# Optimization experiments

Hardware: AMD Instinct MI355X
Metric: run time of the kernel (lower is better)

The kernel has to match this reference:

```python
import jax, jax.numpy as jnp
import numpy as np

# DCNV3_YOLO config: inc==ouc=128 (no stem_conv), k=3, s=1, pad=autopad(3)=1, g=4, d=1, SiLU act
N, C, H, W = 4, 128, 96, 96
G = 4
GC = C // G          # group channels = 32
K = 3                # dcn kernel (also depthwise conv kernel)
PAD = 1
P = K * K            # sampling points per group
EPS = 1e-5


def setup_inputs() -> dict:
    key = jax.random.key(0)
    ks = jax.random.split(key, 8)
    d = {}
    d["x"] = jax.random.normal(ks[0], (N, C, H, W), jnp.float32)
    # DCNv3 params (torch Linear weight (out,in) -> stored transposed (in,out) here)
    d["dw_w"] = jax.random.normal(ks[1], (C, 1, K, K), jnp.float32) * 0.1  # depthwise conv
    d["dw_b"] = jnp.zeros((C,), jnp.float32)
    d["ln_g"] = jnp.ones((C,), jnp.float32)   # LN inside dw_conv branch
    d["ln_b"] = jnp.zeros((C,), jnp.float32)
    d["w_off"] = jax.random.normal(ks[2], (C, G * P * 2), jnp.float32) * 0.01
    d["b_off"] = jnp.zeros((G * P * 2,), jnp.float32)
    d["w_mask"] = jax.random.normal(ks[3], (C, G * P), jnp.float32) * 0.02
    d["b_mask"] = jnp.zeros((G * P,), jnp.float32)
    d["w_in"] = jax.random.normal(ks[4], (C, C), jnp.float32) * (1.0 / np.sqrt(C))
    d["b_in"] = jnp.zeros((C,), jnp.float32)
    d["w_out"] = jax.random.normal(ks[5], (C, C), jnp.float32) * (1.0 / np.sqrt(C))
    d["b_out"] = jnp.zeros((C,), jnp.float32)
    # BatchNorm2d (eval mode: running stats)
    d["bn_g"] = jnp.ones((C,), jnp.float32)
    d["bn_b"] = jnp.zeros((C,), jnp.float32)
    d["bn_mean"] = jnp.zeros((C,), jnp.float32)
    d["bn_var"] = jnp.ones((C,), jnp.float32)
    return d


def _dcnv3_core(xp, offset, mask):
    # xp: (N,H,W,C) projected input; offset: (N,H,W,G*P*2); mask: (N,H,W,G,P) softmaxed
    n, h, w, _ = xp.shape
    xpad = jnp.pad(xp, ((0, 0), (PAD, PAD), (PAD, PAD), (0, 0)))
    H_in, W_in = h + 2 * PAD, w + 2 * PAD
    Ho, Wo = h, w  # stride 1, k=3, pad=1 -> same spatial size
    # reference points (pixel centers in padded frame, normalized), matches _get_reference_points
    base = (K - 1) // 2 + 0.5  # 1.5
    ref_y = (jnp.arange(Ho, dtype=jnp.float32) + base) / H_in
    ref_x = (jnp.arange(Wo, dtype=jnp.float32) + base) / W_in
    # dilation grid; torch flattens meshgrid(x_lin, y_lin) ij -> x outer, y inner
    lin = jnp.arange(K, dtype=jnp.float32) - (K - 1) // 2  # [-1,0,1]
    gx, gy = jnp.meshgrid(lin, lin, indexing='ij')  # (K,K), x varies along axis 0
    gridx = (gx / W_in).reshape(P)
    gridy = (gy / H_in).reshape(P)
    off = offset.reshape(n, Ho, Wo, G, P, 2)
    # normalized sampling locations (offset_scale = 1.0)
    loc_x = ref_x[None, None, :, None, None] + gridx[None, None, None, None, :] + off[..., 0] / W_in
    loc_y = ref_y[None, :, None, None, None] + gridy[None, None, None, None, :] + off[..., 1] / H_in
    # grid_sample(align_corners=False) unnormalize of (2*loc-1): loc*size - 0.5
    ix = (loc_x * W_in - 0.5).transpose(0, 3, 1, 2, 4)  # (N,G,Ho,Wo,P)
    iy = (loc_y * H_in - 0.5).transpose(0, 3, 1, 2, 4)
    x0 = jnp.floor(ix); y0 = jnp.floor(iy)
    wx1 = ix - x0; wx0 = 1.0 - wx1
    wy1 = iy - y0; wy0 = 1.0 - wy1
    x0i = x0.astype(jnp.int32); y0i = y0.astype(jnp.int32)
    x1i = x0i + 1; y1i = y0i + 1
    img = xpad.reshape(n, H_in * W_in, G, GC).transpose(0, 2, 1, 3)  # (N,G,S,GC)

    def samp(yi, xi, wgt):
        valid = (yi >= 0) & (yi < H_in) & (xi >= 0) & (xi < W_in)  # zeros padding
        idx = jnp.clip(yi, 0, H_in - 1) * W_in + jnp.clip(xi, 0, W_in - 1)
        idxf = idx.reshape(n, G, Ho * Wo * P, 1)
        v = jnp.take_along_axis(img, idxf, axis=2)  # (N,G,Ho*Wo*P,GC)
        w_eff = jnp.where(valid, wgt, 0.0).reshape(n, G, Ho * Wo * P, 1)
        return v * w_eff

    val = (samp(y0i, x0i, wy0 * wx0) + samp(y0i, x1i, wy0 * wx1)
           + samp(y1i, x0i, wy1 * wx0) + samp(y1i, x1i, wy1 * wx1))
    val = val.reshape(n, G, Ho, Wo, P, GC)
    m = mask.transpose(0, 3, 1, 2, 4)[..., None]  # (N,G,Ho,Wo,P,1)
    out = (val * m).sum(axis=4)  # (N,G,Ho,Wo,GC)
    return out.transpose(0, 2, 3, 1, 4).reshape(n, Ho, Wo, G * GC)


def reference(x, dw_w, dw_b, ln_g, ln_b, w_off, b_off, w_mask, b_mask,
              w_in, b_in, w_out, b_out, bn_g, bn_b, bn_mean, bn_var):
    x_nhwc = x.transpose(0, 2, 3, 1)  # NCHW -> NHWC
    x_proj = x_nhwc @ w_in + b_in     # input_proj
    # dw_conv branch: depthwise conv -> LayerNorm(channels_last) -> GELU
    x1 = jax.lax.conv_general_dilated(x, dw_w, (1, 1), ((PAD, PAD), (PAD, PAD)),
                                      feature_group_count=C,
                                      dimension_numbers=('NCHW', 'OIHW', 'NCHW'))
    x1 = x1.transpose(0, 2, 3, 1) + dw_b
    mu = x1.mean(-1, keepdims=True)
    var = ((x1 - mu) ** 2).mean(-1, keepdims=True)
    x1 = (x1 - mu) * jax.lax.rsqrt(var + EPS) * ln_g + ln_b
    x1 = jax.nn.gelu(x1, approximate=False)
    offset = x1 @ w_off + b_off  # (N,H,W,G*P*2)
    mask = jax.nn.softmax((x1 @ w_mask + b_mask).reshape(N, H, W, G, P), axis=-1)
    out = _dcnv3_core(x_proj, offset, mask)
    out = out @ w_out + b_out    # output_proj
    y = out.transpose(0, 3, 1, 2)  # back to NCHW
    # BatchNorm2d (eval) + SiLU
    inv = jax.lax.rsqrt(bn_var + EPS)
    y = (y - bn_mean[:, None, None]) * (inv * bn_g)[:, None, None] + bn_b[:, None, None]
    return y * jax.nn.sigmoid(y)
```

## Files before the change

kernel.cpp:

```cpp
#include <hip/hip_runtime.h>
#include <math.h>

#define NN 4
#define CCH 128
#define HH 96
#define WW 96
#define SS (HH*WW)
#define GG 4
#define GC 32
#define PP 9
#define NPIX (NN*HH*WW)

typedef short bf16x8 __attribute__((ext_vector_type(8)));
typedef float f32x4 __attribute__((ext_vector_type(4)));
typedef unsigned short u16;
typedef unsigned int u32;

static __device__ __forceinline__ u16 f2bf(float f) {
  unsigned u = __builtin_bit_cast(unsigned, f);
  unsigned r = (u + 0x7fffu + ((u >> 16) & 1u)) >> 16;
  return (u16)r;
}
static __device__ __forceinline__ float bflo(u32 u) {
  return __builtin_bit_cast(float, u << 16);
}
static __device__ __forceinline__ float bfhi(u32 u) {
  return __builtin_bit_cast(float, u & 0xffff0000u);
}

__global__ __launch_bounds__(128) void k_prep(const float* __restrict__ w_in,
    const float* __restrict__ w_off, const float* __restrict__ w_mask,
    const float* __restrict__ w_out, const float* __restrict__ dw_w,
    u16* __restrict__ w_inT, u16* __restrict__ w_omT, u16* __restrict__ w_outT,
    u16* __restrict__ dw_wT) {
  int r = blockIdx.x, k = threadIdx.x;
  if (r < 128) {
    w_inT[r*128 + k] = f2bf(w_in[k*128 + r]);
  } else if (r < 240) {
    int c = r - 128;
    float v = 0.f;
    if (c < 72) v = w_off[k*72 + c];
    else if (c < 108) v = w_mask[k*36 + (c - 72)];
    w_omT[c*128 + k] = f2bf(v);
  } else if (r < 368) {
    int c = r - 240;
    w_outT[c*128 + k] = f2bf(w_out[k*128 + c]);
  } else {
    int j = r - 368;
    dw_wT[j*128 + k] = f2bf(dw_w[k*9 + j]);
  }
}

__global__ __launch_bounds__(256) void k_tr_in(const float* __restrict__ x,
                                               u16* __restrict__ xTb) {
  __shared__ float tile[32][132];
  int n = blockIdx.z;
  int cs = blockIdx.y * 32;
  int ps = blockIdx.x * 128;
  int t = threadIdx.x;
  const float* src = x + ((size_t)n*CCH + cs)*SS + ps;
  #pragma unroll
  for (int i = 0; i < 4; ++i) {
    int f = t + i*256;
    int row = f >> 5, col4 = f & 31;
    float4 v = *(const float4*)(src + (size_t)row*SS + col4*4);
    *(float4*)&tile[row][col4*4] = v;
  }
  __syncthreads();
  u16* dst = xTb + ((size_t)n*SS + ps)*CCH + cs;
  #pragma unroll
  for (int i = 0; i < 8; ++i) {
    int gidx = t + i*256;
    int px = gidx >> 4, cp = gidx & 15;
    u32 pk = (u32)f2bf(tile[cp*2][px]) | ((u32)f2bf(tile[cp*2+1][px]) << 16);
    *(u32*)(dst + (size_t)px*CCH + cp*2) = pk;
  }
}

__global__ __launch_bounds__(64) void k_proj16(const u16* __restrict__ xTb,
    const u16* __restrict__ wT, const float* __restrict__ bias,
    u16* __restrict__ xpb) {
  int l = threadIdx.x;
  int c16 = l & 15, kq = l >> 4;
  int px0 = blockIdx.x * 16;
  const u16* arow = xTb + (size_t)(px0 + c16)*CCH + kq*8;
  bf16x8 a[4];
  #pragma unroll
  for (int ks = 0; ks < 4; ++ks) a[ks] = *(const bf16x8*)(arow + ks*32);
  f32x4 acc[8] = {};
  #pragma unroll
  for (int ks = 0; ks < 4; ++ks) {
    #pragma unroll
    for (int nt = 0; nt < 8; ++nt) {
      bf16x8 b = *(const bf16x8*)(wT + (size_t)(nt*16 + c16)*CCH + ks*32 + kq*8);
      acc[nt] = __builtin_amdgcn_mfma_f32_16x16x32_bf16(a[ks], b, acc[nt], 0, 0, 0);
    }
  }
  #pragma unroll
  for (int nt = 0; nt < 8; ++nt) {
    int c = nt*16 + c16;
    float bs = bias[c];
    #pragma unroll
    for (int r = 0; r < 4; ++r)
      xpb[(size_t)(px0 + kq*4 + r)*CCH + c] = f2bf(acc[nt][r] + bs);
  }
}

__global__ __launch_bounds__(256) void k_dwom(const u16* __restrict__ xTb,
    const u16* __restrict__ dw_wT, const float* __restrict__ dw_b,
    const float* __restrict__ ln_g, const float* __restrict__ ln_b,
    const u16* __restrict__ wTom, const float* __restrict__ b_off,
    const float* __restrict__ b_mask,
    float* __restrict__ off, float* __restrict__ mask) {
  __shared__ u16 x1t[16][136];
  __shared__ float msk[16][40];
  int t = threadIdx.x;
  int blk = blockIdx.x;
  const int W16 = WW/16;
  int w0 = (blk % W16) * 16;
  int h  = (blk / W16) % HH;
  int n  = blk / (W16*HH);
  size_t pix0 = (size_t)n*SS + (size_t)h*WW + w0;

  {
    int px = t >> 4, cg = t & 15;
    int w = w0 + px;
    int c0 = cg * 8;
    const u16* src = xTb + (size_t)n*SS*CCH + c0;
    float wtv[9][8];
    #pragma unroll
    for (int j = 0; j < 9; ++j) {
      bf16x8 wr = *(const bf16x8*)(dw_wT + j*CCH + c0);
      u32 uw[4]; *(bf16x8*)uw = wr;
      #pragma unroll
      for (int q = 0; q < 4; ++q) { wtv[j][2*q] = bflo(uw[q]); wtv[j][2*q+1] = bfhi(uw[q]); }
    }
    float s8[8] = {};
    #pragma unroll
    for (int kh = 0; kh < 3; ++kh) {
      int yy = h - 1 + kh;
      if (yy < 0 || yy >= HH) continue;
      #pragma unroll
      for (int kw = 0; kw < 3; ++kw) {
        int xx = w - 1 + kw;
        if (xx < 0 || xx >= WW) continue;
        bf16x8 raw = *(const bf16x8*)(src + (size_t)(yy*WW + xx)*CCH);
        u32 uw[4]; *(bf16x8*)uw = raw;
        #pragma unroll
        for (int q = 0; q < 4; ++q) {
          s8[2*q]   = fmaf(bflo(uw[q]), wtv[kh*3+kw][2*q],   s8[2*q]);
          s8[2*q+1] = fmaf(bfhi(uw[q]), wtv[kh*3+kw][2*q+1], s8[2*q+1]);
        }
      }
    }
    float4 db0 = *(const float4*)(dw_b + c0);
    float4 db1 = *(const float4*)(dw_b + c0 + 4);
    s8[0]+=db0.x; s8[1]+=db0.y; s8[2]+=db0.z; s8[3]+=db0.w;
    s8[4]+=db1.x; s8[5]+=db1.y; s8[6]+=db1.z; s8[7]+=db1.w;
    float s1 = 0.f, s2 = 0.f;
    #pragma unroll
    for (int j = 0; j < 8; ++j) { s1 += s8[j]; s2 += s8[j]*s8[j]; }
    #pragma unroll
    for (int m = 8; m >= 1; m >>= 1) {
      s1 += __shfl_xor(s1, m);
      s2 += __shfl_xor(s2, m);
    }
    float mean = s1 * (1.f/128.f);
    float var  = s2 * (1.f/128.f) - mean*mean;
    float rstd = rsqrtf(var + 1e-5f);
    float4 lg0 = *(const float4*)(ln_g + c0);
    float4 lg1 = *(const float4*)(ln_g + c0 + 4);
    float4 lb0 = *(const float4*)(ln_b + c0);
    float4 lb1 = *(const float4*)(ln_b + c0 + 4);
    float lg[8] = {lg0.x,lg0.y,lg0.z,lg0.w,lg1.x,lg1.y,lg1.z,lg1.w};
    float lb[8] = {lb0.x,lb0.y,lb0.z,lb0.w,lb1.x,lb1.y,lb1.z,lb1.w};
    u32 pk[4];
    #pragma unroll
    for (int q = 0; q < 4; ++q) {
      float v0 = (s8[2*q]   - mean) * rstd * lg[2*q]   + lb[2*q];
      float v1 = (s8[2*q+1] - mean) * rstd * lg[2*q+1] + lb[2*q+1];
      float g0 = 0.5f * v0 * (1.f + erff(v0 * 0.70710678f));
      float g1 = 0.5f * v1 * (1.f + erff(v1 * 0.70710678f));
      pk[q] = (u32)f2bf(g0) | ((u32)f2bf(g1) << 16);
    }
    *(bf16x8*)&x1t[px][c0] = *(bf16x8*)pk;
  }
  __syncthreads();

  {
    int wv = t >> 6, l = t & 63, c16 = l & 15, kq = l >> 4;
    int nt0 = wv*2;
    int ntn = (wv == 3) ? 1 : 2;
    f32x4 acc[2] = {};
    #pragma unroll
    for (int ks = 0; ks < 4; ++ks) {
      bf16x8 a = *(const bf16x8*)&x1t[c16][kq*8 + ks*32];
      #pragma unroll
      for (int j = 0; j < 2; ++j) {
        if (j < ntn) {
          bf16x8 b = *(const bf16x8*)(wTom + (size_t)((nt0+j)*16 + c16)*CCH + ks*32 + kq*8);
          acc[j] = __builtin_amdgcn_mfma_f32_16x16x32_bf16(a, b, acc[j], 0, 0, 0);
        }
      }
    }
    #pragma unroll
    for (int j = 0; j < 2; ++j) {
      if (j < ntn) {
        int c = (nt0+j)*16 + c16;
        float bs = (c < 72) ? b_off[c] : ((c < 108) ? b_mask[c - 72] : 0.f);
        #pragma unroll
        for (int r = 0; r < 4; ++r) {
          int px = kq*4 + r;
          float v = acc[j][r] + bs;
          if (c < 72) off[(pix0 + px)*72 + c] = v;
          else if (c < 108) msk[px][c - 72] = v;
        }
      }
    }
  }
  __syncthreads();

  if (t < 64) {
    int px = t >> 2, g = t & 3;
    float mx = -1e30f;
    #pragma unroll
    for (int q = 0; q < PP; ++q) mx = fmaxf(mx, msk[px][g*PP + q]);
    float e[PP]; float sum = 0.f;
    #pragma unroll
    for (int q = 0; q < PP; ++q) { e[q] = __expf(msk[px][g*PP + q] - mx); sum += e[q]; }
    float inv = 1.f / sum;
    #pragma unroll
    for (int q = 0; q < PP; ++q)
      mask[(pix0 + px)*36 + g*PP + q] = e[q] * inv;
  }
}

__global__ __launch_bounds__(256) void k_dcnout(const u16* __restrict__ xpb,
    const float* __restrict__ off, const float* __restrict__ mask,
    const u16* __restrict__ wTout, const float* __restrict__ b_out,
    const float* __restrict__ bn_g, const float* __restrict__ bn_b,
    const float* __restrict__ bn_mean, const float* __restrict__ bn_var,
    float* __restrict__ y) {
  __shared__ float smem[16*132];
  __shared__ u16 dtile[16][136];
  float (*offs)[72] = (float(*)[72])smem;
  float (*ms)[36]   = (float(*)[36])(smem + 16*72);
  int t = threadIdx.x;
  int pb = blockIdx.x * 16;
  {
    const float* po = off + (size_t)pb*72;
    #pragma unroll
    for (int i = 0; i < 5; ++i) {
      int idx = t + i*256;
      if (idx < 16*72) smem[idx] = po[idx];
    }
    const float* pm = mask + (size_t)pb*36;
    #pragma unroll
    for (int i = 0; i < 3; ++i) {
      int idx = t + i*256;
      if (idx < 16*36) smem[16*72 + idx] = pm[idx];
    }
  }
  __syncthreads();

  {
    int pxl = t >> 4, unit = t & 15;
    int g = unit >> 2, ch0 = unit * 8;
    int pix = pb + pxl;
    int w = pix % WW; int h = (pix / WW) % HH; int n = pix / SS;
    const u16* basep = xpb + (size_t)n*SS*CCH + ch0;
    float a8[8] = {};
    #pragma unroll
    for (int bt = 0; bt < 3; ++bt) {
      bf16x8 raw[3][4];
      float wgt[3][4];
      float mv[3];
      #pragma unroll
      for (int q = 0; q < 3; ++q) {
        int p = bt*3 + q;
        float offx = offs[pxl][(g*PP + p)*2 + 0];
        float offy = offs[pxl][(g*PP + p)*2 + 1];
        mv[q] = ms[pxl][g*PP + p];
        float ix = (float)w + 1.0f + (float)(p / 3 - 1) + offx;
        float iy = (float)h + 1.0f + (float)(p % 3 - 1) + offy;
        float x0f = floorf(ix), y0f = floorf(iy);
        float wx1 = ix - x0f, wx0 = 1.f - wx1;
        float wy1 = iy - y0f, wy0 = 1.f - wy1;
        int x0i = (int)x0f, y0i = (int)y0f;
        int ox0 = x0i - 1, oy0 = y0i - 1;
        int ox1 = x0i,     oy1 = y0i;
        bool y0ok = (oy0 >= 0) & (oy0 < HH), y1ok = (oy1 >= 0) & (oy1 < HH);
        bool x0ok = (ox0 >= 0) & (ox0 < WW), x1ok = (ox1 >= 0) & (ox1 < WW);
        int cy0 = min(max(oy0, 0), HH-1), cy1 = min(max(oy1, 0), HH-1);
        int cx0 = min(max(ox0, 0), WW-1), cx1 = min(max(ox1, 0), WW-1);
        wgt[q][0] = (y0ok & x0ok) ? wy0*wx0 : 0.f;
        wgt[q][1] = (y0ok & x1ok) ? wy0*wx1 : 0.f;
        wgt[q][2] = (y1ok & x0ok) ? wy1*wx0 : 0.f;
        wgt[q][3] = (y1ok & x1ok) ? wy1*wx1 : 0.f;
        raw[q][0] = *(const bf16x8*)(basep + (size_t)(cy0*WW + cx0)*CCH);
        raw[q][1] = *(const bf16x8*)(basep + (size_t)(cy0*WW + cx1)*CCH);
        raw[q][2] = *(const bf16x8*)(basep + (size_t)(cy1*WW + cx0)*CCH);
        raw[q][3] = *(const bf16x8*)(basep + (size_t)(cy1*WW + cx1)*CCH);
      }
      #pragma unroll
      for (int q = 0; q < 3; ++q) {
        float v8[8] = {};
        #pragma unroll
        for (int corner = 0; corner < 4; ++corner) {
          u32 uw[4]; *(bf16x8*)uw = raw[q][corner];
          float wg = wgt[q][corner];
          #pragma unroll
          for (int j = 0; j < 4; ++j) {
            v8[2*j]   = fmaf(wg, bflo(uw[j]), v8[2*j]);
            v8[2*j+1] = fmaf(wg, bfhi(uw[j]), v8[2*j+1]);
          }
        }
        #pragma unroll
        for (int j = 0; j < 8; ++j) a8[j] = fmaf(mv[q], v8[j], a8[j]);
      }
    }
    u32 pk[4];
    #pragma unroll
    for (int j = 0; j < 4; ++j)
      pk[j] = (u32)f2bf(a8[2*j]) | ((u32)f2bf(a8[2*j+1]) << 16);
    *(bf16x8*)&dtile[pxl][ch0] = *(bf16x8*)pk;
  }
  __syncthreads();

  {
    int wv = t >> 6, l = t & 63, c16 = l & 15, kq = l >> 4;
    f32x4 acc[2] = {};
    #pragma unroll
    for (int ks = 0; ks < 4; ++ks) {
      bf16x8 a = *(const bf16x8*)&dtile[c16][kq*8 + ks*32];
      #pragma unroll
      for (int j = 0; j < 2; ++j) {
        int nt = wv*2 + j;
        bf16x8 b = *(const bf16x8*)(wTout + (size_t)(nt*16 + c16)*CCH + ks*32 + kq*8);
        acc[j] = __builtin_amdgcn_mfma_f32_16x16x32_bf16(a, b, acc[j], 0, 0, 0);
      }
    }
    float (*fout)[132] = (float(*)[132])smem;
    #pragma unroll
    for (int j = 0; j < 2; ++j) {
      int c = (wv*2 + j)*16 + c16;
      float sc = rsqrtf(bn_var[c] + 1e-5f) * bn_g[c];
      float sh = bn_b[c] - bn_mean[c] * sc;
      float bs = b_out[c];
      #pragma unroll
      for (int r = 0; r < 4; ++r) {
        int px = kq*4 + r;
        float v = (acc[j][r] + bs) * sc + sh;
        float sig = 1.f / (1.f + __expf(-v));
        fout[px][c] = v * sig;
      }
    }
  }
  __syncthreads();

  {
    float (*fout)[132] = (float(*)[132])smem;
    int n = pb / SS, rem = pb % SS;
    float* dst = y + ((size_t)n*CCH)*SS + rem;
    #pragma unroll
    for (int i = 0; i < 2; ++i) {
      int id = t + i*256;
      int c = id >> 2, p4 = (id & 3) * 4;
      float4 v = { fout[p4][c], fout[p4+1][c], fout[p4+2][c], fout[p4+3][c] };
      *(float4*)(dst + (size_t)c*SS + p4) = v;
    }
  }
}

extern "C" void kernel_launch(void* const* d_in, const int* in_sizes, int n_in,
                              void* d_out, int out_size, void* d_ws, size_t ws_size,
                              hipStream_t stream) {
  const float* x       = (const float*)d_in[0];
  const float* dw_w    = (const float*)d_in[1];
  const float* dw_b    = (const float*)d_in[2];
  const float* ln_g    = (const float*)d_in[3];
  const float* ln_b    = (const float*)d_in[4];
  const float* w_off   = (const float*)d_in[5];
  const float* b_off   = (const float*)d_in[6];
  const float* w_mask  = (const float*)d_in[7];
  const float* b_mask  = (const float*)d_in[8];
  const float* w_in    = (const float*)d_in[9];
  const float* b_in    = (const float*)d_in[10];
  const float* w_out   = (const float*)d_in[11];
  const float* b_out   = (const float*)d_in[12];
  const float* bn_g    = (const float*)d_in[13];
  const float* bn_b    = (const float*)d_in[14];
  const float* bn_mean = (const float*)d_in[15];
  const float* bn_var  = (const float*)d_in[16];
  float* y = (float*)d_out;

  u16*  xTb  = (u16*)d_ws;
  u16*  xpb  = xTb + (size_t)NPIX*CCH;
  float* offb = (float*)(xpb + (size_t)NPIX*CCH);
  float* mb   = offb + (size_t)NPIX*72;
  u16*  wbuf  = (u16*)(mb + (size_t)NPIX*36);
  u16*  w_inT  = wbuf;
  u16*  w_omT  = w_inT + 128*128;
  u16*  w_outT = w_omT + 112*128;
  u16*  dw_wTb = w_outT + 128*128;

  dim3 trg(SS/128, CCH/32, NN);
  k_prep<<<377, 128, 0, stream>>>(w_in, w_off, w_mask, w_out, dw_w,
                                  w_inT, w_omT, w_outT, dw_wTb);
  k_tr_in<<<trg, 256, 0, stream>>>(x, xTb);
  k_proj16<<<NPIX/16, 64, 0, stream>>>(xTb, w_inT, b_in, xpb);
  k_dwom<<<NPIX/16, 256, 0, stream>>>(xTb, dw_wTb, dw_b, ln_g, ln_b,
                                      w_omT, b_off, b_mask, offb, mb);
  k_dcnout<<<NPIX/16, 256, 0, stream>>>(xpb, offb, mb, w_outT, b_out,
                                        bn_g, bn_b, bn_mean, bn_var, y);
}
```

Before: 179.3 us.

## Stage a 5x20 halo tile of projected input in LDS for bilinear sampling

```diff
diff --git a/kernel.cpp b/kernel.cpp
--- a/kernel.cpp
+++ b/kernel.cpp
@@ -243,10 +243,15 @@
     float* __restrict__ y) {
   __shared__ float smem[16*132];
   __shared__ u16 dtile[16][136];
+  __shared__ u16 halo[5*20*128];
   float (*offs)[72] = (float(*)[72])smem;
   float (*ms)[36]   = (float(*)[36])(smem + 16*72);
   int t = threadIdx.x;
   int pb = blockIdx.x * 16;
+  int n = pb / SS, rem = pb % SS;
+  int h = rem / WW, w0 = rem % WW;
+  const u16* xpimg = xpb + (size_t)n*SS*CCH;
+
   {
     const float* po = off + (size_t)pb*72;
     #pragma unroll
@@ -260,63 +265,64 @@
       int idx = t + i*256;
       if (idx < 16*36) smem[16*72 + idx] = pm[idx];
     }
+    for (int i = t; i < 1600; i += 256) {
+      int pxl = i >> 4, seg = i & 15;
+      int r = pxl / 20, c = pxl - r*20;
+      int gy = min(max(h - 2 + r, 0), HH-1);
+      int gx = min(max(w0 - 2 + c, 0), WW-1);
+      *(bf16x8*)&halo[(size_t)i*8] =
+          *(const bf16x8*)(xpimg + (size_t)(gy*WW + gx)*CCH + seg*8);
+    }
   }
   __syncthreads();
 
   {
     int pxl = t >> 4, unit = t & 15;
     int g = unit >> 2, ch0 = unit * 8;
-    int pix = pb + pxl;
-    int w = pix % WW; int h = (pix / WW) % HH; int n = pix / SS;
-    const u16* basep = xpb + (size_t)n*SS*CCH + ch0;
+    int w = w0 + pxl;
     float a8[8] = {};
     #pragma unroll
-    for (int bt = 0; bt < 3; ++bt) {
-      bf16x8 raw[3][4];
-      float wgt[3][4];
-      float mv[3];
-      #pragma unroll
-      for (int q = 0; q < 3; ++q) {
-        int p = bt*3 + q;
-        float offx = offs[pxl][(g*PP + p)*2 + 0];
-        float offy = offs[pxl][(g*PP + p)*2 + 1];
-        mv[q] = ms[pxl][g*PP + p];
-        float ix = (float)w + 1.0f + (float)(p / 3 - 1) + offx;
-        float iy = (float)h + 1.0f + (float)(p % 3 - 1) + offy;
-        float x0f = floorf(ix), y0f = floorf(iy);
-        float wx1 = ix - x0f, wx0 = 1.f - wx1;
-        float wy1 = iy - y0f, wy0 = 1.f - wy1;
-        int x0i = (int)x0f, y0i = (int)y0f;
-        int ox0 = x0i - 1, oy0 = y0i - 1;
-        int ox1 = x0i,     oy1 = y0i;
-        bool y0ok = (oy0 >= 0) & (oy0 < HH), y1ok = (oy1 >= 0) & (oy1 < HH);
-        bool x0ok = (ox0 >= 0) & (ox0 < WW), x1ok = (ox1 >= 0) & (ox1 < WW);
-        int cy0 = min(max(oy0, 0), HH-1), cy1 = min(max(oy1, 0), HH-1);
-        int cx0 = min(max(ox0, 0), WW-1), cx1 = min(max(ox1, 0), WW-1);
-        wgt[q][0] = (y0ok & x0ok) ? wy0*wx0 : 0.f;
-        wgt[q][1] = (y0ok & x1ok) ? wy0*wx1 : 0.f;
-        wgt[q][2] = (y1ok & x0ok) ? wy1*wx0 : 0.f;
-        wgt[q][3] = (y1ok & x1ok) ? wy1*wx1 : 0.f;
-        raw[q][0] = *(const bf16x8*)(basep + (size_t)(cy0*WW + cx0)*CCH);
-        raw[q][1] = *(const bf16x8*)(basep + (size_t)(cy0*WW + cx1)*CCH);
-        raw[q][2] = *(const bf16x8*)(basep + (size_t)(cy1*WW + cx0)*CCH);
-        raw[q][3] = *(const bf16x8*)(basep + (size_t)(cy1*WW + cx1)*CCH);
-      }
-      #pragma unroll
-      for (int q = 0; q < 3; ++q) {
-        float v8[8] = {};
+    for (int p = 0; p < PP; ++p) {
+      float offx = offs[pxl][(g*PP + p)*2 + 0];
+      float offy = offs[pxl][(g*PP + p)*2 + 1];
+      float mval = ms[pxl][g*PP + p];
+      float ix = (float)w + 1.0f + (float)(p / 3 - 1) + offx;
+      float iy = (float)h + 1.0f + (float)(p % 3 - 1) + offy;
+      float x0f = floorf(ix), y0f = floorf(iy);
+      float wx1 = ix - x0f, wx0 = 1.f - wx1;
+      float wy1 = iy - y0f, wy0 = 1.f - wy1;
+      int x0i = (int)x0f, y0i = (int)y0f;
+      int ox0 = x0i - 1, oy0 = y0i - 1;
+      int ox1 = x0i,     oy1 = y0i;
+      bool y0ok = (oy0 >= 0) & (oy0 < HH), y1ok = (oy1 >= 0) & (oy1 < HH);
+      bool x0ok = (ox0 >= 0) & (ox0 < WW), x1ok = (ox1 >= 0) & (ox1 < WW);
+      float cw[4];
+      cw[0] = ((y0ok & x0ok) ? wy0*wx0 : 0.f) * mval;
+      cw[1] = ((y0ok & x1ok) ? wy0*wx1 : 0.f) * mval;
+      cw[2] = ((y1ok & x0ok) ? wy1*wx0 : 0.f) * mval;
+      cw[3] = ((y1ok & x1ok) ? wy1*wx1 : 0.f) * mval;
+      int ly0 = oy0 - h + 2, lx0 = ox0 - w0 + 2;
+      #pragma unroll
+      for (int corner = 0; corner < 4; ++corner) {
+        int ly = ly0 + (corner >> 1);
+        int lx = lx0 + (corner & 1);
+        float wg = cw[corner];
+        bf16x8 raw;
+        if ((u32)ly < 5u && (u32)lx < 20u) {
+          raw = *(const bf16x8*)&halo[(size_t)(ly*20 + lx)*128 + ch0];
+        } else {
+          int oy = (corner < 2) ? oy0 : oy0 + 1;
+          int ox = (corner & 1) ? ox0 + 1 : ox0;
+          int cy = min(max(oy, 0), HH-1);
+          int cx = min(max(ox, 0), WW-1);
+          raw = *(const bf16x8*)(xpimg + (size_t)(cy*WW + cx)*CCH + ch0);
+        }
+        u32 uw[4]; *(bf16x8*)uw = raw;
         #pragma unroll
-        for (int corner = 0; corner < 4; ++corner) {
-          u32 uw[4]; *(bf16x8*)uw = raw[q][corner];
-          float wg = wgt[q][corner];
-          #pragma unroll
-          for (int j = 0; j < 4; ++j) {
-            v8[2*j]   = fmaf(wg, bflo(uw[j]), v8[2*j]);
-            v8[2*j+1] = fmaf(wg, bfhi(uw[j]), v8[2*j+1]);
-          }
+        for (int j = 0; j < 4; ++j) {
+          a8[2*j]   = fmaf(wg, bflo(uw[j]), a8[2*j]);
+          a8[2*j+1] = fmaf(wg, bfhi(uw[j]), a8[2*j+1]);
         }
-        #pragma unroll
-        for (int j = 0; j < 8; ++j) a8[j] = fmaf(mv[q], v8[j], a8[j]);
       }
     }
     u32 pk[4];
@@ -360,7 +366,6 @@
 
   {
     float (*fout)[132] = (float(*)[132])smem;
-    int n = pb / SS, rem = pb % SS;
     float* dst = y + ((size_t)n*CCH)*SS + rem;
     #pragma unroll
     for (int i = 0; i < 2; ++i) {
```

After: 194.6 us. 8.5% more time.

## Fuse NCHW transpose with input projection GEMM and fold mask into bilinear weights

Applied to the files above, without the earlier changes.

```diff
diff --git a/kernel.cpp b/kernel.cpp
--- a/kernel.cpp
+++ b/kernel.cpp
@@ -51,58 +51,63 @@
   }
 }
 
-__global__ __launch_bounds__(256) void k_tr_in(const float* __restrict__ x,
-                                               u16* __restrict__ xTb) {
-  __shared__ float tile[32][132];
-  int n = blockIdx.z;
-  int cs = blockIdx.y * 32;
-  int ps = blockIdx.x * 128;
+__global__ __launch_bounds__(256) void k_trproj(const float* __restrict__ x,
+    const u16* __restrict__ wT, const float* __restrict__ bias,
+    u16* __restrict__ xTb, u16* __restrict__ xpb) {
+  __shared__ u16 tile[32][136];
   int t = threadIdx.x;
-  const float* src = x + ((size_t)n*CCH + cs)*SS + ps;
+  int pb = blockIdx.x * 32;
+  int n = pb / SS, ps = pb % SS;
+  const float* src = x + ((size_t)n*CCH)*SS + ps;
+
   #pragma unroll
   for (int i = 0; i < 4; ++i) {
-    int f = t + i*256;
-    int row = f >> 5, col4 = f & 31;
-    float4 v = *(const float4*)(src + (size_t)row*SS + col4*4);
-    *(float4*)&tile[row][col4*4] = v;
-  }
-  __syncthreads();
-  u16* dst = xTb + ((size_t)n*SS + ps)*CCH + cs;
-  #pragma unroll
-  for (int i = 0; i < 8; ++i) {
-    int gidx = t + i*256;
-    int px = gidx >> 4, cp = gidx & 15;
-    u32 pk = (u32)f2bf(tile[cp*2][px]) | ((u32)f2bf(tile[cp*2+1][px]) << 16);
-    *(u32*)(dst + (size_t)px*CCH + cp*2) = pk;
-  }
-}
-
-__global__ __launch_bounds__(64) void k_proj16(const u16* __restrict__ xTb,
-    const u16* __restrict__ wT, const float* __restrict__ bias,
-    u16* __restrict__ xpb) {
-  int l = threadIdx.x;
-  int c16 = l & 15, kq = l >> 4;
-  int px0 = blockIdx.x * 16;
-  const u16* arow = xTb + (size_t)(px0 + c16)*CCH + kq*8;
-  bf16x8 a[4];
-  #pragma unroll
-  for (int ks = 0; ks < 4; ++ks) a[ks] = *(const bf16x8*)(arow + ks*32);
-  f32x4 acc[8] = {};
-  #pragma unroll
-  for (int ks = 0; ks < 4; ++ks) {
-    #pragma unroll
-    for (int nt = 0; nt < 8; ++nt) {
-      bf16x8 b = *(const bf16x8*)(wT + (size_t)(nt*16 + c16)*CCH + ks*32 + kq*8);
-      acc[nt] = __builtin_amdgcn_mfma_f32_16x16x32_bf16(a[ks], b, acc[nt], 0, 0, 0);
-    }
-  }
-  #pragma unroll
-  for (int nt = 0; nt < 8; ++nt) {
-    int c = nt*16 + c16;
-    float bs = bias[c];
-    #pragma unroll
-    for (int r = 0; r < 4; ++r)
-      xpb[(size_t)(px0 + kq*4 + r)*CCH + c] = f2bf(acc[nt][r] + bs);
+    int fid = t + i*256;
+    int c = fid >> 3, q = fid & 7;
+    float4 v = *(const float4*)(src + (size_t)c*SS + q*4);
+    int px = q*4;
+    tile[px+0][c] = f2bf(v.x);
+    tile[px+1][c] = f2bf(v.y);
+    tile[px+2][c] = f2bf(v.z);
+    tile[px+3][c] = f2bf(v.w);
+  }
+  __syncthreads();
+
+  {
+    u32* dst = (u32*)(xTb + (size_t)pb*CCH);
+    #pragma unroll
+    for (int i = 0; i < 8; ++i) {
+      int gidx = t + i*256;
+      int px = gidx >> 6, cp = gidx & 63;
+      dst[(size_t)px*64 + cp] = *(const u32*)&tile[px][cp*2];
+    }
+  }
+
+  {
+    int wv = t >> 6, l = t & 63, c16 = l & 15, kq = l >> 4;
+    int pxl0 = (wv & 1) * 16;
+    int nt0 = (wv >> 1) * 4;
+    bf16x8 a[4];
+    #pragma unroll
+    for (int ks = 0; ks < 4; ++ks)
+      a[ks] = *(const bf16x8*)&tile[pxl0 + c16][kq*8 + ks*32];
+    f32x4 acc[4] = {};
+    #pragma unroll
+    for (int ks = 0; ks < 4; ++ks) {
+      #pragma unroll
+      for (int j = 0; j < 4; ++j) {
+        bf16x8 b = *(const bf16x8*)(wT + (size_t)((nt0+j)*16 + c16)*CCH + ks*32 + kq*8);
+        acc[j] = __builtin_amdgcn_mfma_f32_16x16x32_bf16(a[ks], b, acc[j], 0, 0, 0);
+      }
+    }
+    #pragma unroll
+    for (int j = 0; j < 4; ++j) {
+      int c = (nt0+j)*16 + c16;
+      float bs = bias[c];
+      #pragma unroll
+      for (int r = 0; r < 4; ++r)
+        xpb[(size_t)(pb + pxl0 + kq*4 + r)*CCH + c] = f2bf(acc[j][r] + bs);
+    }
   }
 }
 
@@ -274,13 +279,12 @@
     for (int bt = 0; bt < 3; ++bt) {
       bf16x8 raw[3][4];
       float wgt[3][4];
-      float mv[3];
       #pragma unroll
       for (int q = 0; q < 3; ++q) {
         int p = bt*3 + q;
         float offx = offs[pxl][(g*PP + p)*2 + 0];
         float offy = offs[pxl][(g*PP + p)*2 + 1];
-        mv[q] = ms[pxl][g*PP + p];
+        float mval = ms[pxl][g*PP + p];
         float ix = (float)w + 1.0f + (float)(p / 3 - 1) + offx;
         float iy = (float)h + 1.0f + (float)(p % 3 - 1) + offy;
         float x0f = floorf(ix), y0f = floorf(iy);
@@ -293,10 +297,10 @@
         bool x0ok = (ox0 >= 0) & (ox0 < WW), x1ok = (ox1 >= 0) & (ox1 < WW);
         int cy0 = min(max(oy0, 0), HH-1), cy1 = min(max(oy1, 0), HH-1);
         int cx0 = min(max(ox0, 0), WW-1), cx1 = min(max(ox1, 0), WW-1);
-        wgt[q][0] = (y0ok & x0ok) ? wy0*wx0 : 0.f;
-        wgt[q][1] = (y0ok & x1ok) ? wy0*wx1 : 0.f;
-        wgt[q][2] = (y1ok & x0ok) ? wy1*wx0 : 0.f;
-        wgt[q][3] = (y1ok & x1ok) ? wy1*wx1 : 0.f;
+        wgt[q][0] = ((y0ok & x0ok) ? wy0*wx0 : 0.f) * mval;
+        wgt[q][1] = ((y0ok & x1ok) ? wy0*wx1 : 0.f) * mval;
+        wgt[q][2] = ((y1ok & x0ok) ? wy1*wx0 : 0.f) * mval;
+        wgt[q][3] = ((y1ok & x1ok) ? wy1*wx1 : 0.f) * mval;
         raw[q][0] = *(const bf16x8*)(basep + (size_t)(cy0*WW + cx0)*CCH);
         raw[q][1] = *(const bf16x8*)(basep + (size_t)(cy0*WW + cx1)*CCH);
         raw[q][2] = *(const bf16x8*)(basep + (size_t)(cy1*WW + cx0)*CCH);
@@ -304,19 +308,16 @@
       }
       #pragma unroll
       for (int q = 0; q < 3; ++q) {
-        float v8[8] = {};
         #pragma unroll
         for (int corner = 0; corner < 4; ++corner) {
           u32 uw[4]; *(bf16x8*)uw = raw[q][corner];
           float wg = wgt[q][corner];
           #pragma unroll
           for (int j = 0; j < 4; ++j) {
-            v8[2*j]   = fmaf(wg, bflo(uw[j]), v8[2*j]);
-            v8[2*j+1] = fmaf(wg, bfhi(uw[j]), v8[2*j+1]);
+            a8[2*j]   = fmaf(wg, bflo(uw[j]), a8[2*j]);
+            a8[2*j+1] = fmaf(wg, bfhi(uw[j]), a8[2*j+1]);
           }
         }
-        #pragma unroll
-        for (int j = 0; j < 8; ++j) a8[j] = fmaf(mv[q], v8[j], a8[j]);
       }
     }
     u32 pk[4];
@@ -404,11 +405,9 @@
   u16*  w_outT = w_omT + 112*128;
   u16*  dw_wTb = w_outT + 128*128;
 
-  dim3 trg(SS/128, CCH/32, NN);
   k_prep<<<377, 128, 0, stream>>>(w_in, w_off, w_mask, w_out, dw_w,
                                   w_inT, w_omT, w_outT, dw_wTb);
-  k_tr_in<<<trg, 256, 0, stream>>>(x, xTb);
-  k_proj16<<<NPIX/16, 64, 0, stream>>>(xTb, w_inT, b_in, xpb);
+  k_trproj<<<NPIX/32, 256, 0, stream>>>(x, w_inT, b_in, xTb, xpb);
   k_dwom<<<NPIX/16, 256, 0, stream>>>(xTb, dw_wTb, dw_b, ln_g, ln_b,
                                       w_omT, b_off, b_mask, offb, mb);
   k_dcnout<<<NPIX/16, 256, 0, stream>>>(xpb, offb, mb, w_outT, b_out,
```

Measured after the change: 171.9 us. -4.1%, faster.
